# Kernel optimization log

Measured on AMD Instinct MI355X. Metric: run time of the kernel, lower is better.

Reference implementation:

```python
import jax, jax.numpy as jnp
import numpy as np

B, C, H, W = 2, 48, 128, 256
HEADS = 3
EPS_LN = 1e-6
EPS_NRM = 1e-12


def _conv(x, w, b, padding=0, dilation=1, groups=1):
    # x: NCHW, w: OIHW
    out = jax.lax.conv_general_dilated(
        x, w, window_strides=(1, 1),
        padding=[(padding, padding), (padding, padding)],
        rhs_dilation=(dilation, dilation),
        feature_group_count=groups,
        dimension_numbers=('NCHW', 'OIHW', 'NCHW'))
    return out + b[None, :, None, None]


def _ln2d(x, w, b):
    # LayerNorm over channel dim per pixel (NAFNet-style LayerNorm2d)
    mu = x.mean(axis=1, keepdims=True)
    var = ((x - mu) ** 2).mean(axis=1, keepdims=True)
    return (x - mu) / jnp.sqrt(var + EPS_LN) * w[None, :, None, None] + b[None, :, None, None]


def _l2norm(x):
    # F.normalize(dim=-1): x / max(||x||_2, eps)
    n = jnp.sqrt((x * x).sum(-1, keepdims=True))
    return x / jnp.maximum(n, EPS_NRM)


def setup_inputs() -> dict:
    key = jax.random.key(0)
    ks = iter(jax.random.split(key, 40))
    def nrm(shape, s=0.02):
        return jax.random.normal(next(ks), shape, jnp.float32) * s
    d = {
        'x_l': jax.random.normal(next(ks), (B, C, H, W), jnp.float32),
        'x_r': jax.random.normal(next(ks), (B, C, H, W), jnp.float32),
        'ln1_w': jnp.ones((C,), jnp.float32), 'ln1_b': jnp.zeros((C,), jnp.float32),
        'ln2_w': jnp.ones((C,), jnp.float32), 'ln2_b': jnp.zeros((C,), jnp.float32),
        'qkv_l_w': nrm((3 * C, C, 1, 1)), 'qkv_l_b': jnp.zeros((3 * C,), jnp.float32),
        'qkv_r_w': nrm((3 * C, C, 1, 1)), 'qkv_r_b': jnp.zeros((3 * C,), jnp.float32),
        'dw_l_w': nrm((3 * C, 1, 3, 3)), 'dw_l_b': jnp.zeros((3 * C,), jnp.float32),
        'dw_r_w': nrm((3 * C, 1, 3, 3)), 'dw_r_b': jnp.zeros((3 * C,), jnp.float32),
        'dil0_w': nrm((2 * C, 2 * C, 3, 3)), 'dil0_b': jnp.zeros((2 * C,), jnp.float32),
        'dil1_w': nrm((2 * C, 2 * C, 3, 3)), 'dil1_b': jnp.zeros((2 * C,), jnp.float32),
        'dil2_w': nrm((2 * C, 2 * C, 3, 3)), 'dil2_b': jnp.zeros((2 * C,), jnp.float32),
        'convQ_w': nrm((C, 6 * C, 1, 1)), 'convQ_b': jnp.zeros((C,), jnp.float32),
        'conv1_w': nrm((C, C, 1, 1)), 'conv1_b': jnp.zeros((C,), jnp.float32),
        'conv2_w': nrm((C, C, 1, 1)), 'conv2_b': jnp.zeros((C,), jnp.float32),
        'temperature': jnp.ones((HEADS, 1, 1), jnp.float32),
    }
    return d


def reference(x_l, x_r, ln1_w, ln1_b, ln2_w, ln2_b,
              qkv_l_w, qkv_l_b, qkv_r_w, qkv_r_b,
              dw_l_w, dw_l_b, dw_r_w, dw_r_b,
              dil0_w, dil0_b, dil1_w, dil1_b, dil2_w, dil2_b,
              convQ_w, convQ_b, conv1_w, conv1_b, conv2_w, conv2_b,
              temperature):
    b, c, h, w = x_l.shape
    hw = h * w
    ch = c // HEADS  # channels per head

    norm_l = _ln2d(x_l, ln1_w, ln1_b)
    norm_r = _ln2d(x_r, ln2_w, ln2_b)

    qkvl = _conv(_conv(norm_l, qkv_l_w, qkv_l_b), dw_l_w, dw_l_b, padding=1, groups=3 * c)
    qkvr = _conv(_conv(norm_r, qkv_r_w, qkv_r_b), dw_r_w, dw_r_b, padding=1, groups=3 * c)
    Q_l, K_l, V_l = jnp.split(qkvl, 3, axis=1)
    Q_r, K_r, V_r = jnp.split(qkvr, 3, axis=1)

    Q = jnp.concatenate((Q_l, Q_r), axis=1)  # [b, 2c, h, w]
    Q = jnp.concatenate((
        _conv(Q, dil0_w, dil0_b, padding=2, dilation=2),
        _conv(Q, dil1_w, dil1_b, padding=4, dilation=4),
        _conv(Q, dil2_w, dil2_b, padding=6, dilation=6)), axis=1)  # [b, 6c, h, w]
    Q = _conv(Q, convQ_w, convQ_b)  # [b, c, h, w]

    def heads(t):
        return t.reshape(b, HEADS, ch, hw)

    Q = _l2norm(heads(Q))
    K_l = _l2norm(heads(K_l))
    K_r = _l2norm(heads(K_r))
    V_l = heads(V_l)
    V_r = heads(V_r)

    # channel attention: [b, head, ch, ch]
    A_r2l = jax.nn.softmax(jnp.einsum('bhcn,bhdn->bhcd', Q, K_r) * temperature, axis=-1)
    A_l2r = jax.nn.softmax(jnp.einsum('bhcn,bhdn->bhcd', Q, K_l) * temperature, axis=-1)

    F_l = jnp.einsum('bhcd,bhdn->bhcn', A_r2l, V_l).reshape(b, c, h, w)
    F_r = jnp.einsum('bhcd,bhdn->bhcn', A_l2r, V_r).reshape(b, c, h, w)

    F_l = _conv(F_l, conv1_w, conv1_b)
    F_r = _conv(F_r, conv2_w, conv2_b)
    return (x_l + F_l, x_r + F_r)
```

## Files before the change

kernel.cpp:

```cpp
#include <hip/hip_runtime.h>
#include <hip/hip_bf16.h>

typedef __hip_bfloat16 bf16;
typedef __attribute__((ext_vector_type(8))) short short8;
typedef __attribute__((ext_vector_type(4))) float f32x4;
typedef unsigned int u32;

constexpr int IMG_H = 128;
constexpr int IMG_W = 256;
constexpr int HW    = IMG_H * IMG_W;
constexpr int BB    = 2;
constexpr int CC    = 48;
constexpr int C3    = 144;
constexpr int XPW   = 268;
constexpr int XOFF  = 6;
constexpr int QCP   = 104;
constexpr int QCS   = XPW * QCP;
constexpr int QCH   = QCS / 2;
constexpr int QCCH  = QCS / 8;

constexpr int WO_QKVL_W = 0;
constexpr int WO_QKVR_W = 6912;
constexpr int WO_DWL_W  = 13824;
constexpr int WO_DWR_W  = 15120;
constexpr int WO_C1_W   = 16416;
constexpr int WO_C2_W   = 18720;
constexpr int WO_QKVL_B = 21024;
constexpr int WO_QKVR_B = 21168;
constexpr int WO_DWL_B  = 21312;
constexpr int WO_DWR_B  = 21456;
constexpr int WO_C1_B   = 21600;
constexpr int WO_C2_B   = 21648;
constexpr int WO_LN1W   = 21696;
constexpr int WO_LN1B   = 21744;
constexpr int WO_LN2W   = 21792;
constexpr int WO_LN2B   = 21840;
constexpr int WO_TEMP   = 21888;
constexpr int WO_WQ     = 21952;
constexpr int WO_D0W    = 35776;
constexpr int WO_D1W    = 118720;
constexpr int WO_D2W    = 201664;
constexpr int WO_BQ     = 284608;
constexpr int WO_B0     = 284656;
constexpr int WO_B1     = 284752;
constexpr int WO_B2     = 284848;
constexpr int WO_WPACK  = 284944;
constexpr int WO_EFFB   = 409360;
constexpr int WO_AR2L   = 409712;
constexpr int WO_AL2R   = 411248;
constexpr int WO_M1     = 412800;
constexpr int WO_M2     = 417408;
constexpr int WO_WQP    = 422016;
constexpr int WO_PART   = 431232;
constexpr int WO_PART2  = WO_D0W;

constexpr size_t ACT_BASE_BYTES = 2118144;

constexpr size_t A_P  = 0;
constexpr size_t A_Q1 = 9437184;
constexpr size_t A_Q2 = 18874368;
constexpr size_t A_QC = 28311552;

struct PrepArgs {
  const void* src[25];
  int dst[25];
  int n[25];
};

__device__ __forceinline__ bool probe_bf16(const void* ln1w) {
  return ((const unsigned short*)ln1w)[0] == 0x3F80;
}

__global__ __launch_bounds__(256) void prep_k(PrepArgs a, float* __restrict__ wsf) {
  bool isb = probe_bf16(a.src[12]);
  int t = blockIdx.y;
  int i = blockIdx.x * 256 + threadIdx.x;
  if (i < a.n[t]) {
    float v = isb ? __bfloat162float(((const bf16*)a.src[t])[i])
                  : ((const float*)a.src[t])[i];
    wsf[a.dst[t] + i] = v;
  }
}

__global__ __launch_bounds__(512) void effw2_k(const float* __restrict__ wsf,
                                               bf16* __restrict__ wpack) {
  int d  = blockIdx.x / 96;
  int ci = blockIdx.x % 96;
  __shared__ float wds[864];
  __shared__ float wqs[48 * 97];
  const int wdb = (d == 0) ? WO_D0W : (d == 1) ? WO_D1W : WO_D2W;
  for (int idx = threadIdx.x; idx < 864; idx += 512) {
    int m = idx / 9, tt = idx % 9;
    wds[idx] = wsf[wdb + (m * 96 + ci) * 9 + tt];
  }
  for (int idx = threadIdx.x; idx < 4608; idx += 512) {
    int co = idx / 96, m = idx % 96;
    wqs[co * 97 + m] = wsf[WO_WQ + co * 288 + d * 96 + m];
  }
  __syncthreads();
  int tco = threadIdx.x;
  if (tco < 432) {
    int t = tco / 48, co = tco % 48;
    float s = 0.f;
#pragma unroll 8
    for (int m = 0; m < 96; ++m) s += wqs[co * 97 + m] * wds[m * 9 + t];
    int trow = t / 3, dxi = t % 3;
    int ti = (trow == 0) ? (2 - d) * 3 + dxi
           : (trow == 1) ? 9 + d * 3 + dxi
                         : 18 + d * 3 + dxi;
    int kc = ci >> 5, j = ci & 7;
    int L = ((ci & 31) >> 3) * 16 + (co & 15);
    int nt = co >> 4;
    int f = (ti * 3 + kc) * 3 + nt;
    wpack[(size_t)f * 512 + L * 8 + j] = __float2bfloat16(s);
  }
}

__global__ __launch_bounds__(256) void wqp_k(const float* __restrict__ wsf,
                                             bf16* __restrict__ wqp,
                                             float* __restrict__ effb) {
  if (blockIdx.x == 72) {
    int co = threadIdx.x;
    if (co < 48) {
      float s = wsf[WO_BQ + co];
      for (int m = 0; m < 96; ++m) {
        s += wsf[WO_WQ + co * 288 + m]       * wsf[WO_B0 + m];
        s += wsf[WO_WQ + co * 288 + 96 + m]  * wsf[WO_B1 + m];
        s += wsf[WO_WQ + co * 288 + 192 + m] * wsf[WO_B2 + m];
      }
      effb[co] = s;
    }
    return;
  }
  int idx = blockIdx.x * 256 + threadIdx.x;
  if (idx >= 18432) return;
  int side = idx / 9216;
  int rem = idx % 9216;
  int nt = rem / 1024;
  int kt = (rem / 512) % 2;
  int e  = rem % 512;
  int L = e >> 3, j = e & 7;
  int o = nt * 16 + (L & 15);
  int kp = kt * 32 + (L >> 4) * 8 + j;
  int g = kp >> 4, r = kp & 15;
  float val = 0.f;
  if (r < 12) {
    int c = g * 12 + r;
    val = wsf[(side ? WO_QKVR_W : WO_QKVL_W) + o * 48 + c];
  }
  wqp[idx] = __float2bfloat16(val);
}

__global__ __launch_bounds__(256) void lnqkv_k(
    const void* __restrict__ x, const void* __restrict__ probe,
    const float* __restrict__ lnw, const float* __restrict__ lnb,
    const bf16* __restrict__ wqp_side, const float* __restrict__ qb,
    bf16* __restrict__ pre) {
  __shared__ __align__(16) unsigned char LDSU[21504 + 18432];
  bf16* XNs = (bf16*)LDSU;
  float2* red = (float2*)(LDSU + 9216);
  bf16* Cs = (bf16*)LDSU;
  bf16* W = (bf16*)(LDSU + 21504);
  int tid = threadIdx.x;
  for (int i = tid; i < 1152; i += 256)
    ((uint4*)W)[i] = ((const uint4*)wqp_side)[i];

  int px = tid & 63;
  int w = tid >> 6;
  int p = blockIdx.x * 64 + px;
  int b = p >> 15;
  int pix = p & (HW - 1);
  size_t base = (size_t)b * CC * HW + pix;
  float v[12];
  if (probe_bf16(probe)) {
    const bf16* xp = (const bf16*)x + base;
#pragma unroll
    for (int c = 0; c < 12; ++c)
      v[c] = __bfloat162float(xp[(size_t)(w * 12 + c) * HW]);
  } else {
    const float* xp = (const float*)x + base;
#pragma unroll
    for (int c = 0; c < 12; ++c) v[c] = xp[(size_t)(w * 12 + c) * HW];
  }
  float s = 0.f, s2 = 0.f;
#pragma unroll
  for (int c = 0; c < 12; ++c) { s += v[c]; s2 += v[c] * v[c]; }
  red[w * 64 + px] = make_float2(s, s2);
  __syncthreads();
  float S = 0.f, S2 = 0.f;
#pragma unroll
  for (int i = 0; i < 4; ++i) {
    float2 r2 = red[i * 64 + px];
    S += r2.x; S2 += r2.y;
  }
  float mu = S * (1.f / 48.f);
  float var = S2 * (1.f / 48.f) - mu * mu;
  float rs = rsqrtf(var + 1e-6f);
  bf16 o16[16];
#pragma unroll
  for (int c = 0; c < 12; ++c)
    o16[c] = __float2bfloat16((v[c] - mu) * rs * lnw[w * 12 + c] + lnb[w * 12 + c]);
#pragma unroll
  for (int c = 12; c < 16; ++c) o16[c] = __float2bfloat16(0.f);
  *(uint4*)(XNs + px * 72 + w * 16) = *(uint4*)(o16);
  *(uint4*)(XNs + px * 72 + w * 16 + 8) = *(uint4*)(o16 + 8);
  __syncthreads();

  int L = tid & 63;
  int lo = L & 15, hi = L >> 4;
  const bf16* arow = XNs + (size_t)(w * 16 + lo) * 72 + hi * 8;
  short8 a0 = *(const short8*)(arow);
  short8 a1 = *(const short8*)(arow + 32);
  __syncthreads();
#pragma unroll
  for (int nt = 0; nt < 9; ++nt) {
    float bvv = qb[nt * 16 + lo];
    f32x4 acc = {bvv, bvv, bvv, bvv};
    acc = __builtin_amdgcn_mfma_f32_16x16x32_bf16(
        a0, *(const short8*)(W + (nt * 2 + 0) * 512 + L * 8), acc, 0, 0, 0);
    acc = __builtin_amdgcn_mfma_f32_16x16x32_bf16(
        a1, *(const short8*)(W + (nt * 2 + 1) * 512 + L * 8), acc, 0, 0, 0);
#pragma unroll
    for (int r = 0; r < 4; ++r)
      Cs[(nt * 16 + lo) * 66 + w * 16 + hi * 4 + r] = __float2bfloat16(acc[r]);
  }
  __syncthreads();
  int pix0 = (blockIdx.x * 64) & (HW - 1);
#pragma unroll
  for (int pass = 0; pass < 18; ++pass) {
    int o = pass * 8 + (tid >> 5);
    int px2 = (tid & 31) * 2;
    bf16 t2[2];
    t2[0] = Cs[o * 66 + px2];
    t2[1] = Cs[o * 66 + px2 + 1];
    *(unsigned*)(pre + ((size_t)(b * C3 + o)) * HW + pix0 + px2) = *(unsigned*)t2;
  }
}

__global__ __launch_bounds__(256) void dw_k(
    const bf16* __restrict__ in, const float* __restrict__ w9,
    const float* __restrict__ bias, bf16* __restrict__ out) {
  int gid = blockIdx.x;
  int yt = gid & 15;
  int c = (gid >> 4) % C3;
  int b = gid / (16 * C3);
  int ry = threadIdx.x >> 5, xi = threadIdx.x & 31;
  int y = yt * 8 + ry;
  int x0 = xi * 8;
  const bf16* base = in + ((size_t)(b * C3 + c)) * HW;
  float wv[9];
#pragma unroll
  for (int t = 0; t < 9; ++t) wv[t] = w9[c * 9 + t];
  float bz = bias[c];
  float acc[8];
#pragma unroll
  for (int i = 0; i < 8; ++i) acc[i] = bz;
#pragma unroll
  for (int ky = 0; ky < 3; ++ky) {
    int yy = y + ky - 1;
    if ((unsigned)yy >= (unsigned)IMG_H) continue;
    const bf16* row = base + yy * IMG_W + x0;
    uint4 m = *(const uint4*)(row);
    float f[10];
    f[0] = (x0 > 0) ? __bfloat162float(row[-1]) : 0.f;
    f[9] = (x0 + 8 < IMG_W) ? __bfloat162float(row[8]) : 0.f;
    f[1] = __uint_as_float(m.x << 16);
    f[2] = __uint_as_float(m.x & 0xFFFF0000u);
    f[3] = __uint_as_float(m.y << 16);
    f[4] = __uint_as_float(m.y & 0xFFFF0000u);
    f[5] = __uint_as_float(m.z << 16);
    f[6] = __uint_as_float(m.z & 0xFFFF0000u);
    f[7] = __uint_as_float(m.w << 16);
    f[8] = __uint_as_float(m.w & 0xFFFF0000u);
    float w0 = wv[ky * 3], w1 = wv[ky * 3 + 1], w2 = wv[ky * 3 + 2];
#pragma unroll
    for (int i = 0; i < 8; ++i)
      acc[i] += w0 * f[i] + w1 * f[i + 1] + w2 * f[i + 2];
  }
  bf16 o[8];
#pragma unroll
  for (int i = 0; i < 8; ++i) o[i] = __float2bfloat16(acc[i]);
  *(uint4*)(out + ((size_t)(b * C3 + c)) * HW + y * IMG_W + x0) = *(uint4*)o;
}

__global__ __launch_bounds__(256) void qc_k(const bf16* __restrict__ q1,
                                            const bf16* __restrict__ q2,
                                            bf16* __restrict__ qc) {
  int b = blockIdx.x >> 7;
  int y = blockIdx.x & 127;
  int half = blockIdx.y;
  int tid = threadIdx.x;
  int x0 = half * 128;
  int px = tid & 127;
  int cig = tid >> 7;
  __shared__ __align__(16) bf16 T[128][100];
#pragma unroll 8
  for (int k = 0; k < 48; ++k) {
    int ci = cig * 48 + k;
    const bf16* src = (ci < 48)
        ? q1 + (((size_t)(b * C3 + ci)) * IMG_H + y) * IMG_W
        : q2 + (((size_t)(b * C3 + ci - 48)) * IMG_H + y) * IMG_W;
    T[px][ci] = src[x0 + px];
  }
  __syncthreads();
  size_t rowbase = ((size_t)(b * IMG_H + y)) * QCS;
#pragma unroll 1
  for (int i = 0; i < 14; ++i) {
    int e4 = i * 256 + tid;
    if (e4 >= QCH / 4) break;
    int e = e4 * 4 + half * QCH;
    int xp = e / QCP;
    int cin = e % QCP;
    int x = xp - XOFF;
    uint2 val;
    val.x = 0u; val.y = 0u;
    if ((unsigned)x < (unsigned)IMG_W && cin < 96) {
      val = *(const uint2*)(&T[x - x0][cin]);
    }
    *(uint2*)(qc + rowbase + e) = val;
  }
}

__global__ __launch_bounds__(256, 1) void dil_mfma_k(
    const bf16* __restrict__ qc, const bf16* __restrict__ wp,
    const float* __restrict__ effb, bf16* __restrict__ qh) {
  __shared__ __align__(16) unsigned char LDSU[55744];
  bf16* Arow = (bf16*)LDSU;
  float* Cs  = (float*)LDSU;

  int bid = blockIdx.x;
  int xcd = bid & 7;
  int slot = bid >> 3;
  int y = xcd * 16 + (slot & 15);
  int b = slot >> 4;
  int tid = threadIdx.x;
  int L = tid & 63;
  int w = tid >> 6;
  int lo = L & 15, hi = L >> 4;

  f32x4 acc[4][3];
#pragma unroll
  for (int g2 = 0; g2 < 4; ++g2)
#pragma unroll
    for (int nt = 0; nt < 3; ++nt) {
      float bv = effb[nt * 16 + lo];
      acc[g2][nt] = {bv, bv, bv, bv};
    }

  const bf16* wrow = wp + L * 8;
  short8 wc[9];
#pragma unroll
  for (int f = 0; f < 9; ++f)
    wc[f] = *(const short8*)(wrow + f * 512);

  int dy_prev = -100;
#pragma unroll 1
  for (int g = 0; g < 9; ++g) {
    int D = (g < 3) ? (6 - 2 * g) : (g < 6) ? (2 * (g - 2)) : (2 * (g - 5));
    int dy = (g < 3) ? -D : (g < 6) ? 0 : D;
    int yy = y + dy;
    bool valid = (unsigned)yy < (unsigned)IMG_H;
    if (valid && dy != dy_prev) {
      __syncthreads();
      const bf16* src = qc + (size_t)(b * IMG_H + yy) * QCS;
#pragma unroll
      for (int r = 0; r < 14; ++r) {
        int c = w + r * 4;
        int i = c * 64 + L;
        if (i < QCCH) {
          __builtin_amdgcn_global_load_lds(
              (const __attribute__((address_space(1))) u32*)(src + (size_t)i * 8),
              (__attribute__((address_space(3))) u32*)(Arow + (size_t)c * 512),
              16, 0, 0);
        }
      }
      __syncthreads();
      dy_prev = dy;
    }
#pragma unroll
    for (int dxi = 0; dxi < 3; ++dxi) {
      int ti = g * 3 + dxi;
      short8 wn[9];
      if (ti < 26) {
        const bf16* wr = wrow + (ti + 1) * 4608;
#pragma unroll
        for (int f = 0; f < 9; ++f)
          wn[f] = *(const short8*)(wr + f * 512);
      }
      if (valid) {
        int dx = (dxi - 1) * D;
        const bf16* ar = Arow + (size_t)(XOFF + dx + w * 64 + lo) * QCP + hi * 8;
#pragma unroll
        for (int g2 = 0; g2 < 4; ++g2)
#pragma unroll
          for (int kc = 0; kc < 3; ++kc) {
            short8 a = *(const short8*)(ar + g2 * (16 * QCP) + kc * 32);
#pragma unroll
            for (int nt = 0; nt < 3; ++nt)
              acc[g2][nt] = __builtin_amdgcn_mfma_f32_16x16x32_bf16(
                  a, wc[kc * 3 + nt], acc[g2][nt], 0, 0, 0);
          }
      }
      if (ti < 26) {
#pragma unroll
        for (int f = 0; f < 9; ++f) wc[f] = wn[f];
      }
    }
  }

  __syncthreads();
#pragma unroll
  for (int g2 = 0; g2 < 4; ++g2)
#pragma unroll
    for (int nt = 0; nt < 3; ++nt)
#pragma unroll
      for (int r = 0; r < 4; ++r)
        Cs[(nt * 16 + lo) * 260 + w * 64 + g2 * 16 + hi * 4 + r] = acc[g2][nt][r];
  __syncthreads();
  size_t obase = (size_t)b * CC * HW + (size_t)y * IMG_W;
#pragma unroll 1
  for (int i = 0; i < 12; ++i) {
    int chunk = i * 256 + tid;
    int co = chunk >> 6;
    int px4 = (chunk & 63) * 4;
    const float* s = Cs + co * 260 + px4;
    bf16 t4[4];
    t4[0] = __float2bfloat16(s[0]);
    t4[1] = __float2bfloat16(s[1]);
    t4[2] = __float2bfloat16(s[2]);
    t4[3] = __float2bfloat16(s[3]);
    *(uint2*)(qh + obase + (size_t)co * HW + px4) = *(uint2*)t4;
  }
}

__device__ __forceinline__ float blo(unsigned u) {
  return __uint_as_float(u << 16);
}
__device__ __forceinline__ float bhi(unsigned u) {
  return __uint_as_float(u & 0xFFFF0000u);
}

__global__ __launch_bounds__(256) void logits_mfma_k(
    const bf16* __restrict__ qh, const bf16* __restrict__ qkvl,
    const bf16* __restrict__ qkvr, float* __restrict__ part,
    float* __restrict__ part2) {
  int abh = blockIdx.x;
  int chunk = blockIdx.y;
  int a = abh / 6;
  int b = (abh / 3) % 2;
  int h = abh % 3;
  int tid = threadIdx.x;
  int L = tid & 63, w = tid >> 6;
  int lo = L & 15, hi = L >> 4;
  const bf16* qrow = qh + ((size_t)(b * CC + h * 16 + lo)) * HW;
  const bf16* krow =
      ((a == 0) ? qkvr : qkvl) + ((size_t)(b * C3 + 48 + h * 16 + lo)) * HW;
  int px0 = chunk * 1024 + w * 256 + hi * 8;
  f32x4 acc = {0.f, 0.f, 0.f, 0.f};
  float aq = 0.f, ak = 0.f;
#pragma unroll
  for (int s = 0; s < 8; ++s) {
    short8 av = *(const short8*)(qrow + px0 + s * 32);
    short8 bv = *(const short8*)(krow + px0 + s * 32);
    acc = __builtin_amdgcn_mfma_f32_16x16x32_bf16(av, bv, acc, 0, 0, 0);
#pragma unroll
    for (int j = 0; j < 4; ++j) {
      u32 ua = ((const u32*)&av)[j];
      u32 ub = ((const u32*)&bv)[j];
      float q0 = blo(ua), q1 = bhi(ua);
      float k0 = blo(ub), k1 = bhi(ub);
      aq += q0 * q0 + q1 * q1;
      ak += k0 * k0 + k1 * k1;
    }
  }
  __shared__ float red[4][256];
  __shared__ float sq[256], sk[256];
#pragma unroll
  for (int r = 0; r < 4; ++r) red[w][(hi * 4 + r) * 16 + lo] = acc[r];
  sq[tid] = aq;
  sk[tid] = ak;
  __syncthreads();
  float sum = red[0][tid] + red[1][tid] + red[2][tid] + red[3][tid];
  part[((size_t)abh * 32 + chunk) * 256 + tid] = sum;
  if (tid < 32) {
    const float* srcr = (tid < 16) ? sq : sk;
    int lo2 = tid & 15;
    float s = 0.f;
#pragma unroll
    for (int w2 = 0; w2 < 4; ++w2)
#pragma unroll
      for (int h2 = 0; h2 < 4; ++h2) s += srcr[w2 * 64 + h2 * 16 + lo2];
    part2[((size_t)abh * 32 + chunk) * 32 + tid] = s;
  }
}

__global__ __launch_bounds__(256) void logits_red_k(
    const float* __restrict__ part, const float* __restrict__ part2,
    const float* __restrict__ temp, float* __restrict__ logr2l,
    float* __restrict__ logl2r) {
  int abh = blockIdx.x;
  int a = abh / 6, h = abh % 3;
  int bnum = (abh / 3) % 2;
  int t = threadIdx.x;
  int i = t >> 4, j = t & 15;
  __shared__ float nrm[32];
  if (t < 32) {
    float s = 0.f;
    const float* p2 = part2 + (size_t)abh * 32 * 32 + t;
#pragma unroll 8
    for (int c = 0; c < 32; ++c) s += p2[c * 32];
    nrm[t] = fmaxf(sqrtf(s), 1e-12f);
  }
  float s = 0.f;
  const float* p = part + (size_t)abh * 32 * 256 + t;
#pragma unroll 8
  for (int c = 0; c < 32; ++c) s += p[c * 256];
  __syncthreads();
  float val = s / (nrm[i] * nrm[16 + j]) * temp[h];
  ((a == 0) ? logr2l : logl2r)[bnum * 768 + h * 256 + i * 16 + j] = val;
}

__global__ __launch_bounds__(256) void softmaxM_k(float* __restrict__ wsf) {
  int tid = threadIdx.x;
  __shared__ float A1[1536], A2[1536];
  if (tid < 192) {
    const float* p = wsf + ((tid < 96) ? WO_AR2L : WO_AL2R) + (tid % 96) * 16;
    float* dst = ((tid < 96) ? A1 : A2) + (tid % 96) * 16;
    float m = -1e30f;
#pragma unroll
    for (int j = 0; j < 16; ++j) m = fmaxf(m, p[j]);
    float s = 0.f;
    float e[16];
#pragma unroll
    for (int j = 0; j < 16; ++j) {
      e[j] = expf(p[j] - m);
      s += e[j];
    }
    float inv = 1.f / s;
#pragma unroll
    for (int j = 0; j < 16; ++j) dst[j] = e[j] * inv;
  }
  __syncthreads();
#pragma unroll 1
  for (int idx = tid; idx < 4608; idx += 256) {
    int b = idx / 2304;
    int r = idx % 2304;
    int o = r / 48;
    int cp = r % 48;
    int h = cp >> 4, j = cp & 15;
    const float* a1 = &A1[((b * 3 + h) * 16) * 16 + j];
    const float* a2 = &A2[((b * 3 + h) * 16) * 16 + j];
    float s1 = 0.f, s2 = 0.f;
#pragma unroll
    for (int i = 0; i < 16; ++i) {
      s1 += wsf[WO_C1_W + o * 48 + h * 16 + i] * a1[i * 16];
      s2 += wsf[WO_C2_W + o * 48 + h * 16 + i] * a2[i * 16];
    }
    wsf[WO_M1 + idx] = s1;
    wsf[WO_M2 + idx] = s2;
  }
}

__global__ __launch_bounds__(256) void attn_out2_k(
    const bf16* __restrict__ q1, const bf16* __restrict__ q2,
    const void* __restrict__ x1, const void* __restrict__ x2,
    const void* __restrict__ probe, const float* __restrict__ Mall,
    const float* __restrict__ cball, void* __restrict__ out) {
  int side = blockIdx.y;
  const bf16* qkv = side ? q2 : q1;
  const void* x = side ? x2 : x1;
  const float* M = Mall + side * 4608;
  const float* cb = cball + side * 48;
  int tid = threadIdx.x;
  int p = blockIdx.x * 256 + tid;
  int b = __builtin_amdgcn_readfirstlane(p >> 15);
  int pix = p & (HW - 1);
  bool isb = probe_bf16(probe);

  float v[CC];
  const bf16* vb = qkv + ((size_t)(b * C3 + 96)) * HW + pix;
#pragma unroll
  for (int c = 0; c < CC; ++c) v[c] = __bfloat162float(vb[(size_t)c * HW]);

  const float* Mb = M + b * 2304;
  size_t base = (size_t)b * CC * HW + pix;
  size_t obase = (size_t)side * BB * CC * HW + base;
  if (isb) {
    const bf16* xp = (const bf16*)x + base;
    bf16* op = (bf16*)out + obase;
#pragma unroll 4
    for (int o = 0; o < CC; ++o) {
      float acc = cb[o];
      const float* mrow = Mb + o * 48;
#pragma unroll
      for (int c = 0; c < CC; ++c) acc += mrow[c] * v[c];
      op[(size_t)o * HW] =
          __float2bfloat16(acc + __bfloat162float(xp[(size_t)o * HW]));
    }
  } else {
    const float* xp = (const float*)x + base;
    float* op = (float*)out + obase;
#pragma unroll 4
    for (int o = 0; o < CC; ++o) {
      float acc = cb[o];
      const float* mrow = Mb + o * 48;
#pragma unroll
      for (int c = 0; c < CC; ++c) acc += mrow[c] * v[c];
      op[(size_t)o * HW] = acc + xp[(size_t)o * HW];
    }
  }
}

extern "C" void kernel_launch(void* const* d_in, const int* in_sizes, int n_in,
                              void* d_out, int out_size, void* d_ws, size_t ws_size,
                              hipStream_t stream) {
  (void)in_sizes; (void)n_in; (void)out_size; (void)ws_size;
  const void* x_l = d_in[0];
  const void* x_r = d_in[1];
  const void* probe = d_in[2];
  float* wsf = (float*)d_ws;
  bf16* wpack = (bf16*)(wsf + WO_WPACK);
  bf16* wqp = (bf16*)(wsf + WO_WQP);
  bf16* act = (bf16*)((char*)d_ws + ACT_BASE_BYTES);
  bf16* P  = act + A_P;
  bf16* Q1 = act + A_Q1;
  bf16* Q2 = act + A_Q2;
  bf16* QC = act + A_QC;
  bf16* qh = P;

  PrepArgs pa;
  const int srcIdx[25] = {6, 8, 10, 12, 22, 24, 7, 9, 11, 13, 23, 25,
                          2, 3, 4, 5, 26, 20, 14, 16, 18, 21, 15, 17, 19};
  const int dstOff[25] = {WO_QKVL_W, WO_QKVR_W, WO_DWL_W, WO_DWR_W, WO_C1_W, WO_C2_W,
                          WO_QKVL_B, WO_QKVR_B, WO_DWL_B, WO_DWR_B, WO_C1_B, WO_C2_B,
                          WO_LN1W, WO_LN1B, WO_LN2W, WO_LN2B, WO_TEMP,
                          WO_WQ, WO_D0W, WO_D1W, WO_D2W, WO_BQ, WO_B0, WO_B1, WO_B2};
  const int ns[25] = {6912, 6912, 1296, 1296, 2304, 2304, 144, 144, 144, 144,
                      48, 48, 48, 48, 48, 48, 3,
                      13824, 82944, 82944, 82944, 48, 96, 96, 96};
  for (int i = 0; i < 25; ++i) {
    pa.src[i] = d_in[srcIdx[i]];
    pa.dst[i] = dstOff[i];
    pa.n[i] = ns[i];
  }
  prep_k<<<dim3(324, 25), 256, 0, stream>>>(pa, wsf);

  effw2_k<<<288, 512, 0, stream>>>(wsf, wpack);
  wqp_k<<<73, 256, 0, stream>>>(wsf, wqp, wsf + WO_EFFB);

  lnqkv_k<<<1024, 256, 0, stream>>>(x_l, probe, wsf + WO_LN1W, wsf + WO_LN1B,
                                    wqp, wsf + WO_QKVL_B, P);
  dw_k<<<BB * C3 * 16, 256, 0, stream>>>(P, wsf + WO_DWL_W, wsf + WO_DWL_B, Q1);
  lnqkv_k<<<1024, 256, 0, stream>>>(x_r, probe, wsf + WO_LN2W, wsf + WO_LN2B,
                                    wqp + 9216, wsf + WO_QKVR_B, P);
  dw_k<<<BB * C3 * 16, 256, 0, stream>>>(P, wsf + WO_DWR_W, wsf + WO_DWR_B, Q2);

  qc_k<<<dim3(BB * IMG_H, 2), 256, 0, stream>>>(Q1, Q2, QC);

  dil_mfma_k<<<256, 256, 0, stream>>>(QC, wpack, wsf + WO_EFFB, qh);

  logits_mfma_k<<<dim3(12, 32), 256, 0, stream>>>(qh, Q1, Q2, wsf + WO_PART,
                                                  wsf + WO_PART2);
  logits_red_k<<<12, 256, 0, stream>>>(wsf + WO_PART, wsf + WO_PART2,
                                       wsf + WO_TEMP, wsf + WO_AR2L,
                                       wsf + WO_AL2R);
  softmaxM_k<<<1, 256, 0, stream>>>(wsf);

  attn_out2_k<<<dim3(256, 2), 256, 0, stream>>>(
      Q1, Q2, x_l, x_r, probe, wsf + WO_M1, wsf + WO_C1_B, d_out);
}
```

Before: 276.6 us.

## Split dilated conv rows into half-width blocks and compact weight prep grid

The dilated MFMA conv now has each block handle half an image row (128 pixels) instead of a full row. That doubles the grid to 512 blocks, shrinks LDS to about 29 KB and allows two blocks per CU. The prep kernel uses a compact 1D grid with per-tensor chunk offsets instead of a 324x25 grid that was mostly idle blocks. The large dilated weights are no longer copied to workspace and are read directly from the inputs in effw2_k. The trade-off is that each row's shared halo is loaded twice and each block does less work per weight fetch.

```diff
diff --git a/kernel.cpp b/kernel.cpp
--- a/kernel.cpp
+++ b/kernel.cpp
@@ -17,7 +17,6 @@
 constexpr int QCP   = 104;
 constexpr int QCS   = XPW * QCP;
 constexpr int QCH   = QCS / 2;
-constexpr int QCCH  = QCS / 8;
 
 constexpr int WO_QKVL_W = 0;
 constexpr int WO_QKVR_W = 6912;
@@ -38,8 +37,6 @@
 constexpr int WO_TEMP   = 21888;
 constexpr int WO_WQ     = 21952;
 constexpr int WO_D0W    = 35776;
-constexpr int WO_D1W    = 118720;
-constexpr int WO_D2W    = 201664;
 constexpr int WO_BQ     = 284608;
 constexpr int WO_B0     = 284656;
 constexpr int WO_B1     = 284752;
@@ -61,10 +58,12 @@
 constexpr size_t A_Q2 = 18874368;
 constexpr size_t A_QC = 28311552;
 
+constexpr int NPREP = 22;
 struct PrepArgs {
-  const void* src[25];
-  int dst[25];
-  int n[25];
+  const void* src[NPREP];
+  int dst[NPREP];
+  int n[NPREP];
+  int cstart[NPREP];
 };
 
 __device__ __forceinline__ bool probe_bf16(const void* ln1w) {
@@ -73,8 +72,11 @@
 
 __global__ __launch_bounds__(256) void prep_k(PrepArgs a, float* __restrict__ wsf) {
   bool isb = probe_bf16(a.src[12]);
-  int t = blockIdx.y;
-  int i = blockIdx.x * 256 + threadIdx.x;
+  int chunk = blockIdx.x;
+  int t = 0;
+#pragma unroll 1
+  while (t < NPREP - 1 && chunk >= a.cstart[t + 1]) ++t;
+  int i = (chunk - a.cstart[t]) * 256 + threadIdx.x;
   if (i < a.n[t]) {
     float v = isb ? __bfloat162float(((const bf16*)a.src[t])[i])
                   : ((const float*)a.src[t])[i];
@@ -82,16 +84,21 @@
   }
 }
 
-__global__ __launch_bounds__(512) void effw2_k(const float* __restrict__ wsf,
-                                               bf16* __restrict__ wpack) {
+__global__ __launch_bounds__(512) void effw2_k(
+    const float* __restrict__ wsf, const void* __restrict__ dwa,
+    const void* __restrict__ dwb, const void* __restrict__ dwc,
+    const void* __restrict__ probe, bf16* __restrict__ wpack) {
   int d  = blockIdx.x / 96;
   int ci = blockIdx.x % 96;
   __shared__ float wds[864];
   __shared__ float wqs[48 * 97];
-  const int wdb = (d == 0) ? WO_D0W : (d == 1) ? WO_D1W : WO_D2W;
+  const void* dwp = (d == 0) ? dwa : (d == 1) ? dwb : dwc;
+  bool isb = probe_bf16(probe);
   for (int idx = threadIdx.x; idx < 864; idx += 512) {
     int m = idx / 9, tt = idx % 9;
-    wds[idx] = wsf[wdb + (m * 96 + ci) * 9 + tt];
+    int e = (m * 96 + ci) * 9 + tt;
+    wds[idx] = isb ? __bfloat162float(((const bf16*)dwp)[e])
+                   : ((const float*)dwp)[e];
   }
   for (int idx = threadIdx.x; idx < 4608; idx += 512) {
     int co = idx / 96, m = idx % 96;
@@ -321,26 +328,29 @@
   }
 }
 
-__global__ __launch_bounds__(256, 1) void dil_mfma_k(
+__global__ __launch_bounds__(256, 2) void dil_mfma_k(
     const bf16* __restrict__ qc, const bf16* __restrict__ wp,
     const float* __restrict__ effb, bf16* __restrict__ qh) {
-  __shared__ __align__(16) unsigned char LDSU[55744];
+  __shared__ __align__(16) unsigned char LDSU[29120];
   bf16* Arow = (bf16*)LDSU;
   float* Cs  = (float*)LDSU;
+  constexpr int WCH = 140 * QCP / 8;
 
   int bid = blockIdx.x;
   int xcd = bid & 7;
-  int slot = bid >> 3;
-  int y = xcd * 16 + (slot & 15);
-  int b = slot >> 4;
+  int rest = bid >> 3;
+  int y = xcd * 16 + (rest & 15);
+  int half = (rest >> 4) & 1;
+  int b = rest >> 5;
+  int x0 = half * 128;
   int tid = threadIdx.x;
   int L = tid & 63;
   int w = tid >> 6;
   int lo = L & 15, hi = L >> 4;
 
-  f32x4 acc[4][3];
-#pragma unroll
-  for (int g2 = 0; g2 < 4; ++g2)
+  f32x4 acc[2][3];
+#pragma unroll
+  for (int g2 = 0; g2 < 2; ++g2)
 #pragma unroll
     for (int nt = 0; nt < 3; ++nt) {
       float bv = effb[nt * 16 + lo];
@@ -362,12 +372,12 @@
     bool valid = (unsigned)yy < (unsigned)IMG_H;
     if (valid && dy != dy_prev) {
       __syncthreads();
-      const bf16* src = qc + (size_t)(b * IMG_H + yy) * QCS;
-#pragma unroll
-      for (int r = 0; r < 14; ++r) {
+      const bf16* src = qc + (size_t)(b * IMG_H + yy) * QCS + (size_t)x0 * QCP;
+#pragma unroll
+      for (int r = 0; r < 8; ++r) {
         int c = w + r * 4;
         int i = c * 64 + L;
-        if (i < QCCH) {
+        if (i < WCH) {
           __builtin_amdgcn_global_load_lds(
               (const __attribute__((address_space(1))) u32*)(src + (size_t)i * 8),
               (__attribute__((address_space(3))) u32*)(Arow + (size_t)c * 512),
@@ -389,9 +399,9 @@
       }
       if (valid) {
         int dx = (dxi - 1) * D;
-        const bf16* ar = Arow + (size_t)(XOFF + dx + w * 64 + lo) * QCP + hi * 8;
-#pragma unroll
-        for (int g2 = 0; g2 < 4; ++g2)
+        const bf16* ar = Arow + (size_t)(XOFF + dx + w * 32 + lo) * QCP + hi * 8;
+#pragma unroll
+        for (int g2 = 0; g2 < 2; ++g2)
 #pragma unroll
           for (int kc = 0; kc < 3; ++kc) {
             short8 a = *(const short8*)(ar + g2 * (16 * QCP) + kc * 32);
@@ -410,20 +420,20 @@
 
   __syncthreads();
 #pragma unroll
-  for (int g2 = 0; g2 < 4; ++g2)
+  for (int g2 = 0; g2 < 2; ++g2)
 #pragma unroll
     for (int nt = 0; nt < 3; ++nt)
 #pragma unroll
       for (int r = 0; r < 4; ++r)
-        Cs[(nt * 16 + lo) * 260 + w * 64 + g2 * 16 + hi * 4 + r] = acc[g2][nt][r];
-  __syncthreads();
-  size_t obase = (size_t)b * CC * HW + (size_t)y * IMG_W;
-#pragma unroll 1
-  for (int i = 0; i < 12; ++i) {
+        Cs[(nt * 16 + lo) * 132 + w * 32 + g2 * 16 + hi * 4 + r] = acc[g2][nt][r];
+  __syncthreads();
+  size_t obase = (size_t)b * CC * HW + (size_t)y * IMG_W + x0;
+#pragma unroll
+  for (int i = 0; i < 6; ++i) {
     int chunk = i * 256 + tid;
-    int co = chunk >> 6;
-    int px4 = (chunk & 63) * 4;
-    const float* s = Cs + co * 260 + px4;
+    int co = chunk >> 5;
+    int px4 = (chunk & 31) * 4;
+    const float* s = Cs + co * 132 + px4;
     bf16 t4[4];
     t4[0] = __float2bfloat16(s[0]);
     t4[1] = __float2bfloat16(s[1]);
@@ -629,23 +639,26 @@
   bf16* qh = P;
 
   PrepArgs pa;
-  const int srcIdx[25] = {6, 8, 10, 12, 22, 24, 7, 9, 11, 13, 23, 25,
-                          2, 3, 4, 5, 26, 20, 14, 16, 18, 21, 15, 17, 19};
-  const int dstOff[25] = {WO_QKVL_W, WO_QKVR_W, WO_DWL_W, WO_DWR_W, WO_C1_W, WO_C2_W,
-                          WO_QKVL_B, WO_QKVR_B, WO_DWL_B, WO_DWR_B, WO_C1_B, WO_C2_B,
-                          WO_LN1W, WO_LN1B, WO_LN2W, WO_LN2B, WO_TEMP,
-                          WO_WQ, WO_D0W, WO_D1W, WO_D2W, WO_BQ, WO_B0, WO_B1, WO_B2};
-  const int ns[25] = {6912, 6912, 1296, 1296, 2304, 2304, 144, 144, 144, 144,
-                      48, 48, 48, 48, 48, 48, 3,
-                      13824, 82944, 82944, 82944, 48, 96, 96, 96};
-  for (int i = 0; i < 25; ++i) {
+  const int srcIdx[NPREP] = {6, 8, 10, 12, 22, 24, 7, 9, 11, 13, 23, 25,
+                             2, 3, 4, 5, 26, 20, 21, 15, 17, 19};
+  const int dstOff[NPREP] = {WO_QKVL_W, WO_QKVR_W, WO_DWL_W, WO_DWR_W, WO_C1_W,
+                             WO_C2_W, WO_QKVL_B, WO_QKVR_B, WO_DWL_B, WO_DWR_B,
+                             WO_C1_B, WO_C2_B, WO_LN1W, WO_LN1B, WO_LN2W,
+                             WO_LN2B, WO_TEMP, WO_WQ, WO_BQ, WO_B0, WO_B1, WO_B2};
+  const int ns[NPREP] = {6912, 6912, 1296, 1296, 2304, 2304, 144, 144, 144, 144,
+                         48, 48, 48, 48, 48, 48, 3, 13824, 48, 96, 96, 96};
+  int ck = 0;
+  for (int i = 0; i < NPREP; ++i) {
     pa.src[i] = d_in[srcIdx[i]];
     pa.dst[i] = dstOff[i];
     pa.n[i] = ns[i];
-  }
-  prep_k<<<dim3(324, 25), 256, 0, stream>>>(pa, wsf);
-
-  effw2_k<<<288, 512, 0, stream>>>(wsf, wpack);
+    pa.cstart[i] = ck;
+    ck += (ns[i] + 255) / 256;
+  }
+  prep_k<<<ck, 256, 0, stream>>>(pa, wsf);
+
+  effw2_k<<<288, 512, 0, stream>>>(wsf, d_in[14], d_in[16], d_in[18],
+                                   probe, wpack);
   wqp_k<<<73, 256, 0, stream>>>(wsf, wqp, wsf + WO_EFFB);
 
   lnqkv_k<<<1024, 256, 0, stream>>>(x_l, probe, wsf + WO_LN1W, wsf + WO_LN1B,
@@ -657,7 +670,7 @@
 
   qc_k<<<dim3(BB * IMG_H, 2), 256, 0, stream>>>(Q1, Q2, QC);
 
-  dil_mfma_k<<<256, 256, 0, stream>>>(QC, wpack, wsf + WO_EFFB, qh);
+  dil_mfma_k<<<512, 256, 0, stream>>>(QC, wpack, wsf + WO_EFFB, qh);
 
   logits_mfma_k<<<dim3(12, 32), 256, 0, stream>>>(qh, Q1, Q2, wsf + WO_PART,
                                                   wsf + WO_PART2);
```

Result: no change. 277.6 us (+0.4%).
